# Performance work log

Hardware: AMD Instinct MI355X
Metric: run time of the kernel (lower is better)

Reference implementation:

```python
import jax, jax.numpy as jnp
import numpy as np

N_NODE, N_USER = 100000, 30000
N_REL, N_BASIS = 8, 30
EMB, OUT = 32, 32
E = 1600000
BATCH = 16384
H1, H2, H3 = 64, 32, 16
NEG_SLOPE = 0.2


def setup_inputs() -> dict:
    key = jax.random.key(0)
    ks = jax.random.split(key, 20)
    g = lambda k, shape: jax.random.normal(k, shape, dtype=jnp.float32) * 0.05
    inp = {
        "x_ids": jnp.arange(N_NODE, dtype=jnp.int64 if jax.config.jax_enable_x64 else jnp.int32),
        "edge_index": jax.random.randint(ks[0], (2, E), 0, N_NODE),
        "edge_type": jax.random.randint(ks[1], (E,), 0, N_REL),
        "users": jax.random.randint(ks[2], (BATCH,), 0, N_USER),
        "bundles": jax.random.randint(ks[3], (BATCH,), 0, N_NODE),
        # parameters
        "emb": g(ks[4], (N_NODE, EMB)),
        "basis": g(ks[5], (N_BASIS, EMB, OUT)),
        "weight": g(ks[6], (N_REL, N_BASIS)),
        "att": g(ks[7], (N_REL, 2 * OUT)),
        "root": g(ks[8], (EMB, OUT)),
        "bias": jnp.zeros((OUT,), jnp.float32),
        "W1": g(ks[9], (2 * OUT, H1)), "b1": jnp.zeros((H1,), jnp.float32),
        "W2": g(ks[10], (H1, H2)), "b2": jnp.zeros((H2,), jnp.float32),
        "W3": g(ks[11], (H2, H3)), "b3": jnp.zeros((H3,), jnp.float32),
        "Wo": g(ks[12], (H3, 1)), "bo": jnp.zeros((1,), jnp.float32),
    }
    return inp


def _tgcn_fwd(x_ids, edge_index, edge_type, users, bundles,
              emb, basis, weight, att, root, bias,
              W1, b1, W2, b2, W3, b3, Wo, bo):
    N = emb.shape[0]
    R = weight.shape[0]
    O = basis.shape[2]
    x = emb[x_ids]                                   # (N, F) embedding lookup
    # basis decomposition: (R, F, O)
    w = (weight @ basis.reshape(N_BASIS, -1)).reshape(R, EMB, O)
    # transform every node under every relation once, then gather per edge
    xh = jnp.einsum('nf,rfo->nro', x, w)             # (N, R, O)
    src, dst = edge_index[0], edge_index[1]          # j (source), i (target)
    h_i = xh[dst, edge_type]                         # (E, O)
    h_j = xh[src, edge_type]                         # (E, O)
    a = att[edge_type]                               # (E, 2O)
    alpha = (h_i * a[:, :O]).sum(-1) + (h_j * a[:, O:]).sum(-1)
    alpha = jax.nn.leaky_relu(alpha, NEG_SLOPE)
    # segment softmax keyed by (target node, relation)
    seg_key = dst * R + edge_type
    n_seg = N * R
    amax = jax.ops.segment_max(alpha, seg_key, num_segments=n_seg)
    ex = jnp.exp(alpha - amax[seg_key])
    denom = jax.ops.segment_sum(ex, seg_key, num_segments=n_seg)
    alpha = ex / (denom[seg_key] + 1e-16)
    # scatter-add weighted messages into target nodes
    agg = jax.ops.segment_sum(h_j * alpha[:, None], dst, num_segments=N)
    h = jax.nn.relu(agg + x @ root + bias)           # update + ReLU
    z = jnp.concatenate([h[users], h[bundles]], axis=1)  # (B, 2O)
    z = jax.nn.relu(z @ W1 + b1)
    z = jax.nn.relu(z @ W2 + b2)
    z = jax.nn.relu(z @ W3 + b3)
    return z @ Wo + bo                               # (B, 1) logits


def reference(x_ids, edge_index, edge_type, users, bundles,
              emb, basis, weight, att, root, bias,
              W1, b1, W2, b2, W3, b3, Wo, bo):
    return _tgcn_fwd(x_ids, edge_index, edge_type, users, bundles,
                     emb, basis, weight, att, root, bias,
                     W1, b1, W2, b2, W3, b3, Wo, bo)
```

## Files before the change

### kernel.cpp

```cpp
#include <hip/hip_runtime.h>
#include <hip/hip_bf16.h>

#define N_NODE 100000
#define N_REL  8
#define EMB    32
#define OUT    32
#define N_BASIS 30
#define E_EDGE 1600000
#define BATCH  16384
#define H1 64
#define H2 32
#define H3 16
#define NEG_SLOPE 0.2f

#define BSH   8
#define NBKT  391
#define BCAP  5120
#define PCH   2048

#define K5T   64

#define NPB   32
#define NTILES (N_NODE / NPB)
#define K1GRID 782
#define XSS   36
#define RTS   36


struct SortSmem {
    unsigned ent[BCAP];
    unsigned ent2[BCAP];
    unsigned hist[256], dbase[256], dcur[256], sc[256];
};
struct K1Smem {
    float xs[2][NPB * XSS];
    float rootsT[OUT * RTS];
    float was[16 * RTS];
    float biass[OUT];
};

__global__ __launch_bounds__(256) void k0f(const float* __restrict__ weight,
                                           const float* __restrict__ basis,
                                           const float* __restrict__ att,
                                           float* __restrict__ w,
                                           float* __restrict__ wa,
                                           unsigned* __restrict__ bcnt) {
    __shared__ float wl[N_REL * EMB * OUT];
    int t = threadIdx.x;
    for (int i = t; i < N_REL * EMB * OUT; i += 256) {
        int r = i >> 10, fo = i & 1023;
        float acc = 0.f;
        #pragma unroll
        for (int b = 0; b < N_BASIS; b++)
            acc = fmaf(weight[r * N_BASIS + b], basis[b * (EMB * OUT) + fo], acc);
        wl[i] = acc;
        w[i] = acc;
    }
    __syncthreads();
    for (int i = t; i < 512; i += 256) {
        int which = i >> 8, rf = i & 255, r = rf >> 5, f = rf & 31;
        const float* wrow = wl + (r * 32 + f) * 32;
        const float* arow = att + r * 64 + which * 32;
        float acc = 0.f;
        #pragma unroll
        for (int o = 0; o < 32; o++) acc = fmaf(wrow[o], arow[o], acc);
        wa[i] = acc;
    }
    for (int i = t; i < NBKT; i += 256) bcnt[i] = 0;
}

__device__ __forceinline__ void k1x_body(K1Smem& K, int bid0,
                                         const float* __restrict__ emb,
                                         const float* __restrict__ w,
                                         const float* __restrict__ wa,
                                         const float* __restrict__ root,
                                         const float* __restrict__ bias,
                                         unsigned short* __restrict__ xh,
                                         float* __restrict__ p_i,
                                         float* __restrict__ p_j,
                                         float* __restrict__ agg) {
    const int t = threadIdx.x;
    const int ro = t & 127;
    const int rhi = ro >> 5, olo = ro & 31;

    float wc0[EMB], wc1[EMB];
    #pragma unroll
    for (int f = 0; f < EMB; f++) {
        wc0[f] = w[rhi * 1024 + f * 32 + olo];
        wc1[f] = w[rhi * 1024 + 4096 + f * 32 + olo];
    }
    #pragma unroll
    for (int f = 0; f < EMB; f++) asm volatile("" : "+v"(wc0[f]), "+v"(wc1[f]));

    for (int i = t; i < EMB * OUT; i += 256) {
        int f = i >> 5, oo = i & 31;
        K.rootsT[oo * RTS + f] = root[i];
    }
    for (int i = t; i < 512; i += 256) {
        int which = i >> 8, r = (i >> 5) & 7, f = i & 31;
        K.was[(which * 8 + r) * RTS + f] = wa[i];
    }
    if (t < OUT) K.biass[t] = bias[t];

    const int sn = t >> 3, scn = t & 7;
    int tile = bid0;
    {
        float4 v = ((const float4*)(emb + (size_t)tile * NPB * EMB))[t];
        *(float4*)&K.xs[0][sn * XSS + scn * 4] = v;
    }
    __syncthreads();

    int buf = 0;
    for (; tile < NTILES; tile += K1GRID) {
        const int ntile = tile + K1GRID;
        const bool has = ntile < NTILES;
        float4 pf;
        if (has)
            pf = ((const float4*)(emb + (size_t)ntile * NPB * EMB))[t];

        const int n0 = tile * NPB;
        const float* xb = K.xs[buf];

        {
            const float4* xr = (const float4*)&xb[(t >> 3) * XSS];
            const float4* wi = (const float4*)&K.was[(t & 7) * RTS];
            const float4* wj = (const float4*)&K.was[(8 + (t & 7)) * RTS];
            float ai = 0.f, aj = 0.f;
            #pragma unroll
            for (int c = 0; c < 8; c++) {
                float4 xv = xr[c];
                float4 vi = wi[c], vj = wj[c];
                ai = fmaf(xv.x, vi.x, ai); ai = fmaf(xv.y, vi.y, ai);
                ai = fmaf(xv.z, vi.z, ai); ai = fmaf(xv.w, vi.w, ai);
                aj = fmaf(xv.x, vj.x, aj); aj = fmaf(xv.y, vj.y, aj);
                aj = fmaf(xv.z, vj.z, aj); aj = fmaf(xv.w, vj.w, aj);
            }
            p_i[n0 * N_REL + t] = ai;
            p_j[n0 * N_REL + t] = aj;
        }

        {
            const int o = t & 31, ng = t >> 5;
            const float4* rt = (const float4*)&K.rootsT[o * RTS];
            float4 r0 = rt[0], r1 = rt[1], r2 = rt[2], r3 = rt[3];
            float4 r4 = rt[4], r5 = rt[5], r6 = rt[6], r7 = rt[7];
            float bv = K.biass[o];
            #pragma unroll
            for (int q = 0; q < 4; q++) {
                int n = ng * 4 + q;
                const float4* xr = (const float4*)&xb[n * XSS];
                float g = bv;
                float4 xv;
                xv = xr[0]; g = fmaf(xv.x, r0.x, g); g = fmaf(xv.y, r0.y, g);
                            g = fmaf(xv.z, r0.z, g); g = fmaf(xv.w, r0.w, g);
                xv = xr[1]; g = fmaf(xv.x, r1.x, g); g = fmaf(xv.y, r1.y, g);
                            g = fmaf(xv.z, r1.z, g); g = fmaf(xv.w, r1.w, g);
                xv = xr[2]; g = fmaf(xv.x, r2.x, g); g = fmaf(xv.y, r2.y, g);
                            g = fmaf(xv.z, r2.z, g); g = fmaf(xv.w, r2.w, g);
                xv = xr[3]; g = fmaf(xv.x, r3.x, g); g = fmaf(xv.y, r3.y, g);
                            g = fmaf(xv.z, r3.z, g); g = fmaf(xv.w, r3.w, g);
                xv = xr[4]; g = fmaf(xv.x, r4.x, g); g = fmaf(xv.y, r4.y, g);
                            g = fmaf(xv.z, r4.z, g); g = fmaf(xv.w, r4.w, g);
                xv = xr[5]; g = fmaf(xv.x, r5.x, g); g = fmaf(xv.y, r5.y, g);
                            g = fmaf(xv.z, r5.z, g); g = fmaf(xv.w, r5.w, g);
                xv = xr[6]; g = fmaf(xv.x, r6.x, g); g = fmaf(xv.y, r6.y, g);
                            g = fmaf(xv.z, r6.z, g); g = fmaf(xv.w, r6.w, g);
                xv = xr[7]; g = fmaf(xv.x, r7.x, g); g = fmaf(xv.y, r7.y, g);
                            g = fmaf(xv.z, r7.z, g); g = fmaf(xv.w, r7.w, g);
                agg[(size_t)(n0 + n) * OUT + o] = g;
            }
        }

        {
            const int half = t >> 7;
            #pragma unroll 4
            for (int s = 0; s < 16; s++) {
                int n = 2 * s + half;
                const float4* xr = (const float4*)&xb[n * XSS];
                float a0 = 0.f, a1 = 0.f;
                #pragma unroll
                for (int c = 0; c < 8; c++) {
                    float4 xv = xr[c];
                    a0 = fmaf(xv.x, wc0[4 * c + 0], a0);
                    a0 = fmaf(xv.y, wc0[4 * c + 1], a0);
                    a0 = fmaf(xv.z, wc0[4 * c + 2], a0);
                    a0 = fmaf(xv.w, wc0[4 * c + 3], a0);
                    a1 = fmaf(xv.x, wc1[4 * c + 0], a1);
                    a1 = fmaf(xv.y, wc1[4 * c + 1], a1);
                    a1 = fmaf(xv.z, wc1[4 * c + 2], a1);
                    a1 = fmaf(xv.w, wc1[4 * c + 3], a1);
                }
                __hip_bfloat16 b0 = __float2bfloat16(a0);
                __hip_bfloat16 b1 = __float2bfloat16(a1);
                unsigned short* xp = xh + (size_t)(n0 + n) * 256;
                xp[ro]       = *(unsigned short*)&b0;
                xp[ro + 128] = *(unsigned short*)&b1;
            }
        }

        if (has)
            *(float4*)&K.xs[buf ^ 1][sn * XSS + scn * 4] = pf;
        __syncthreads();
        buf ^= 1;
    }
}

__device__ __forceinline__ void sort_body(SortSmem& S, int b,
                                          const unsigned* __restrict__ bcnt,
                                          const unsigned* __restrict__ part,
                                          int* __restrict__ payload,
                                          int* __restrict__ begp,
                                          int* __restrict__ endp) {
    int t = threadIdx.x;
    unsigned s0 = (unsigned)b * BCAP;
    int n = (int)bcnt[b];
    if (n > BCAP) n = BCAP;
    S.hist[t] = 0;
    __syncthreads();
    int n4 = n & ~3;
    for (int i = 4 * t; i < n4; i += 1024) {
        uint4 e4 = *(const uint4*)&part[s0 + i];
        S.ent[i + 0] = e4.x; atomicAdd(&S.hist[e4.x >> 20], 1u);
        S.ent[i + 1] = e4.y; atomicAdd(&S.hist[e4.y >> 20], 1u);
        S.ent[i + 2] = e4.z; atomicAdd(&S.hist[e4.z >> 20], 1u);
        S.ent[i + 3] = e4.w; atomicAdd(&S.hist[e4.w >> 20], 1u);
    }
    for (int i = n4 + t; i < n; i += 256) {
        unsigned e = part[s0 + i];
        S.ent[i] = e;
        atomicAdd(&S.hist[e >> 20], 1u);
    }
    __syncthreads();
    unsigned v = S.hist[t];
    S.sc[t] = v;
    __syncthreads();
    for (int off = 1; off < 256; off <<= 1) {
        unsigned y = (t >= off) ? S.sc[t - off] : 0u;
        __syncthreads();
        S.sc[t] += y;
        __syncthreads();
    }
    unsigned ex = S.sc[t] - v;
    S.dbase[t] = ex;
    S.dcur[t] = ex;
    __syncthreads();
    int d = (b << BSH) + t;
    if (d < N_NODE) {
        begp[d] = (int)(s0 + S.dbase[t]);
        endp[d] = (int)(s0 + S.dbase[t] + S.hist[t]);
    }
    for (int i = t; i < n; i += 256) {
        unsigned e = S.ent[i];
        unsigned pos = atomicAdd(&S.dcur[e >> 20], 1u);
        S.ent2[pos] = e & 0xFFFFFu;
    }
    __syncthreads();
    for (int i = 4 * t; i < n4; i += 1024) {
        uint4 o4 = { S.ent2[i + 0], S.ent2[i + 1], S.ent2[i + 2], S.ent2[i + 3] };
        *(uint4*)&payload[s0 + i] = o4;
    }
    for (int i = n4 + t; i < n; i += 256) payload[s0 + i] = (int)S.ent2[i];
}

__global__ __launch_bounds__(256) void k1x(const float* __restrict__ emb,
                                           const float* __restrict__ w,
                                           const float* __restrict__ wa,
                                           const float* __restrict__ root,
                                           const float* __restrict__ bias,
                                           unsigned short* __restrict__ xh,
                                           float* __restrict__ p_i,
                                           float* __restrict__ p_j,
                                           float* __restrict__ agg) {
    __shared__ K1Smem K;
    k1x_body(K, blockIdx.x, emb, w, wa, root, bias, xh, p_i, p_j, agg);
}

__global__ __launch_bounds__(256) void k_sort(const unsigned* __restrict__ bcnt,
                                              const unsigned* __restrict__ part,
                                              int* __restrict__ payload,
                                              int* __restrict__ begp,
                                              int* __restrict__ endp) {
    __shared__ SortSmem S;
    sort_body(S, blockIdx.x, bcnt, part, payload, begp, endp);
}

__global__ __launch_bounds__(256) void k_sx(const unsigned* __restrict__ bcnt,
                                            const unsigned* __restrict__ part,
                                            int* __restrict__ payload,
                                            int* __restrict__ begp,
                                            int* __restrict__ endp,
                                            const float* __restrict__ emb,
                                            const float* __restrict__ w,
                                            const float* __restrict__ wa,
                                            const float* __restrict__ root,
                                            const float* __restrict__ bias,
                                            unsigned short* __restrict__ xh,
                                            float* __restrict__ p_i,
                                            float* __restrict__ p_j,
                                            float* __restrict__ agg) {
    __shared__ union USmem { SortSmem s; K1Smem k; } u;
    if (blockIdx.x < K1GRID)
        k1x_body(u.k, blockIdx.x, emb, w, wa, root, bias, xh, p_i, p_j, agg);
    else
        sort_body(u.s, blockIdx.x - K1GRID, bcnt, part, payload, begp, endp);
}

__global__ __launch_bounds__(256) void k_part(const int* __restrict__ src,
                                              const int* __restrict__ dst,
                                              const int* __restrict__ et,
                                              unsigned* __restrict__ bcnt,
                                              unsigned* __restrict__ part) {
    __shared__ unsigned long long stage[PCH];
    __shared__ unsigned hist[NBKT], lbase[NBKT], lcur[NBKT], gbase[NBKT];
    __shared__ unsigned sc[256];
    int t = threadIdx.x;
    for (int i = t; i < NBKT; i += 256) hist[i] = 0;
    __syncthreads();
    int beg = blockIdx.x * PCH, end = min(beg + PCH, E_EDGE);
    int n = end - beg;
    int ng = n >> 2;
    int g0 = t, g1 = t + 256;
    bool has0 = g0 < ng, has1 = g1 < ng;
    int4 s0v = {}, d0v = {}, e0v = {}, s1v = {}, d1v = {}, e1v = {};
    if (has0) {
        s0v = *(const int4*)&src[beg + 4 * g0];
        d0v = *(const int4*)&dst[beg + 4 * g0];
        e0v = *(const int4*)&et[beg + 4 * g0];
    }
    if (has1) {
        s1v = *(const int4*)&src[beg + 4 * g1];
        d1v = *(const int4*)&dst[beg + 4 * g1];
        e1v = *(const int4*)&et[beg + 4 * g1];
    }
    if (has0) {
        atomicAdd(&hist[(unsigned)d0v.x >> BSH], 1u);
        atomicAdd(&hist[(unsigned)d0v.y >> BSH], 1u);
        atomicAdd(&hist[(unsigned)d0v.z >> BSH], 1u);
        atomicAdd(&hist[(unsigned)d0v.w >> BSH], 1u);
    }
    if (has1) {
        atomicAdd(&hist[(unsigned)d1v.x >> BSH], 1u);
        atomicAdd(&hist[(unsigned)d1v.y >> BSH], 1u);
        atomicAdd(&hist[(unsigned)d1v.z >> BSH], 1u);
        atomicAdd(&hist[(unsigned)d1v.w >> BSH], 1u);
    }
    __syncthreads();
    unsigned v0 = (2 * t < NBKT) ? hist[2 * t] : 0u;
    unsigned v1 = (2 * t + 1 < NBKT) ? hist[2 * t + 1] : 0u;
    unsigned s = v0 + v1;
    sc[t] = s;
    __syncthreads();
    for (int off = 1; off < 256; off <<= 1) {
        unsigned y = (t >= off) ? sc[t - off] : 0u;
        __syncthreads();
        sc[t] += y;
        __syncthreads();
    }
    unsigned ex = sc[t] - s;
    if (2 * t < NBKT)     { lbase[2 * t] = ex;          lcur[2 * t] = ex; }
    if (2 * t + 1 < NBKT) { lbase[2 * t + 1] = ex + v0; lcur[2 * t + 1] = ex + v0; }
    __syncthreads();
    #define K_PART_STAGE(dd, ss, ee) do {                                   \
        unsigned b_ = (unsigned)(dd) >> BSH;                                \
        unsigned ent_ = ((unsigned)((dd) & 255) << 20)                      \
                      | ((unsigned)(ss) << 3) | (unsigned)(ee);             \
        unsigned pos_ = atomicAdd(&lcur[b_], 1u);                           \
        stage[pos_] = ((unsigned long long)b_ << 32) | ent_; } while (0)
    if (has0) {
        K_PART_STAGE(d0v.x, s0v.x, e0v.x);
        K_PART_STAGE(d0v.y, s0v.y, e0v.y);
        K_PART_STAGE(d0v.z, s0v.z, e0v.z);
        K_PART_STAGE(d0v.w, s0v.w, e0v.w);
    }
    if (has1) {
        K_PART_STAGE(d1v.x, s1v.x, e1v.x);
        K_PART_STAGE(d1v.y, s1v.y, e1v.y);
        K_PART_STAGE(d1v.z, s1v.z, e1v.z);
        K_PART_STAGE(d1v.w, s1v.w, e1v.w);
    }
    #undef K_PART_STAGE
    __syncthreads();
    for (int i = t; i < NBKT; i += 256)
        if (hist[i]) gbase[i] = atomicAdd(&bcnt[i], hist[i]);
    __syncthreads();
    for (int i = t; i < n; i += 256) {
        unsigned long long s64 = stage[i];
        unsigned b = (unsigned)(s64 >> 32);
        unsigned ent = (unsigned)s64;
        part[b * BCAP + gbase[b] + (i - lbase[b])] = ent;
    }
}

__global__ __launch_bounds__(256) void k_agg(const int* __restrict__ begp,
                                             const int* __restrict__ endp,
                                             const int* __restrict__ payload,
                                             const float* __restrict__ p_i,
                                             const float* __restrict__ p_j,
                                             const unsigned short* __restrict__ xh,
                                             float* __restrict__ agg,
                                             int d0, int d1) {
    int d = d0 + blockIdx.x * 4 + (threadIdx.x >> 6);
    if (d >= d1) return;
    const int lane = threadIdx.x & 63;
    const int h = lane >> 5;
    const int o = lane & 31;
    const int beg = begp[d], end = endp[d];
    const int cnt = end - beg;
    if (cnt == 0) return;

    float pid[8];
    #pragma unroll
    for (int k = 0; k < 8; k++) pid[k] = p_i[(d << 3) | k];

    if (cnt <= 64) {
        int sr = 0, r = 0; float ev = 0.f;
        if (lane < cnt) {
            sr = payload[beg + lane];
            r = sr & 7;
            float pi = pid[0];
            #pragma unroll
            for (int k = 1; k < 8; k++) pi = (r == k) ? pid[k] : pi;
            float a = pi + p_j[sr];
            a = (a >= 0.f) ? a : NEG_SLOPE * a;
            ev = __expf(a);
        }
        float sex[8];
        #pragma unroll
        for (int k = 0; k < 8; k++) sex[k] = (r == k) ? ev : 0.f;
        #pragma unroll
        for (int k = 0; k < 8; k++) {
            #pragma unroll
            for (int m = 1; m <= 32; m <<= 1) sex[k] += __shfl_xor(sex[k], m, 64);
        }
        float de = sex[0];
        #pragma unroll
        for (int k = 1; k < 8; k++) de = (r == k) ? sex[k] : de;
        float al = ev / (de + 1e-16f);

        float w0 = 0.f, w1 = 0.f, w2 = 0.f, w3 = 0.f;
        for (int j0 = 0; j0 < cnt; j0 += 8) {
            float b0 = __shfl(al, j0 + h,     64);
            float b1 = __shfl(al, j0 + 2 + h, 64);
            float b2 = __shfl(al, j0 + 4 + h, 64);
            float b3 = __shfl(al, j0 + 6 + h, 64);
            int t0 = payload[beg + j0 + h]     & 0xFFFFF;
            int t1 = payload[beg + j0 + 2 + h] & 0xFFFFF;
            int t2 = payload[beg + j0 + 4 + h] & 0xFFFFF;
            int t3 = payload[beg + j0 + 6 + h] & 0xFFFFF;
            float x0 = __uint_as_float((unsigned)xh[((unsigned)t0 << 5) + o] << 16);
            float x1 = __uint_as_float((unsigned)xh[((unsigned)t1 << 5) + o] << 16);
            float x2 = __uint_as_float((unsigned)xh[((unsigned)t2 << 5) + o] << 16);
            float x3 = __uint_as_float((unsigned)xh[((unsigned)t3 << 5) + o] << 16);
            w0 = fmaf(b0, x0, w0); w1 = fmaf(b1, x1, w1);
            w2 = fmaf(b2, x2, w2); w3 = fmaf(b3, x3, w3);
        }
        float vv = (w0 + w1) + (w2 + w3);
        vv += __shfl_xor(vv, 32, 64);
        if (h == 0) agg[(size_t)d * OUT + o] += vv;
        return;
    }

    float sex[8] = {0.f,0.f,0.f,0.f,0.f,0.f,0.f,0.f};
    for (int i = beg + lane; i < end; i += 64) {
        int sr = payload[i];
        int r = sr & 7;
        float pi = pid[0];
        #pragma unroll
        for (int k = 1; k < 8; k++) pi = (r == k) ? pid[k] : pi;
        float a = pi + p_j[sr];
        a = (a >= 0.f) ? a : NEG_SLOPE * a;
        float ev = __expf(a);
        #pragma unroll
        for (int k = 0; k < 8; k++) sex[k] += (r == k) ? ev : 0.f;
    }
    #pragma unroll
    for (int k = 0; k < 8; k++) {
        #pragma unroll
        for (int m = 1; m <= 32; m <<= 1) sex[k] += __shfl_xor(sex[k], m, 64);
    }
    float v0 = 0.f;
    for (int c = beg; c < end; c += 64) {
        int i = c + lane;
        int sr = 0; float al = 0.f;
        if (i < end) {
            sr = payload[i];
            int r = sr & 7;
            float pi = pid[0];
            #pragma unroll
            for (int k = 1; k < 8; k++) pi = (r == k) ? pid[k] : pi;
            float a = pi + p_j[sr];
            a = (a >= 0.f) ? a : NEG_SLOPE * a;
            float ev = __expf(a);
            float de = sex[0];
            #pragma unroll
            for (int k = 1; k < 8; k++) de = (r == k) ? sex[k] : de;
            al = ev / (de + 1e-16f);
        }
        int m = min(64, end - c);
        for (int j0 = 0; j0 < m; j0 += 2) {
            int e0 = j0 + h;
            float a0 = __shfl(al, e0, 64); int s0 = __shfl(sr, e0, 64);
            if (e0 < m) {
                float xv = __uint_as_float((unsigned)xh[((unsigned)s0 << 5) + o] << 16);
                v0 = fmaf(a0, xv, v0);
            }
        }
    }
    float vv = v0;
    vv += __shfl_xor(vv, 32, 64);
    if (h == 0) agg[(size_t)d * OUT + o] += vv;
}

__global__ __launch_bounds__(K5T, 1) void k5_mlp(const int* __restrict__ users,
                                                 const int* __restrict__ bundles,
                                                 const float* __restrict__ agg,
                                                 const float* __restrict__ W1,
                                                 const float* __restrict__ b1,
                                                 const float* __restrict__ W2,
                                                 const float* __restrict__ b2,
                                                 const float* __restrict__ W3,
                                                 const float* __restrict__ b3,
                                                 const float* __restrict__ Wo,
                                                 const float* __restrict__ bo,
                                                 float* __restrict__ out) {
    __shared__ float4 W1s[2 * OUT * H1 / 4];
    __shared__ float4 W2s[H1 * H2 / 4];
    __shared__ float4 W3s[H2 * H3 / 4];
    __shared__ float b1s[H1], b2s[H2], b3s[H3], Wos[H3];
    __shared__ float bos;
    __shared__ float zs[K5T * 65];
    __shared__ float h1s[K5T * 65];
    const int t = threadIdx.x;

    const float4* W14 = (const float4*)W1;
    const float4* W24 = (const float4*)W2;
    const float4* W34 = (const float4*)W3;
    for (int i = t; i < 1024; i += K5T) W1s[i] = W14[i];
    for (int i = t; i < 512; i += K5T) W2s[i] = W24[i];
    for (int i = t; i < 128; i += K5T) W3s[i] = W34[i];
    if (t < H2) b2s[t] = b2[t];
    if (t < H3) { b3s[t] = b3[t]; Wos[t] = Wo[t]; }
    if (t < H1) b1s[t] = b1[t];
    if (t == 0) bos = bo[0];

    const int item = blockIdx.x * K5T + t;
    const int u = users[item], v = bundles[item];
    const float4* av = (const float4*)agg;
    float* zrow = &zs[t * 65];
    float* h1row = &h1s[t * 65];

    #pragma unroll
    for (int c = 0; c < 8; c++) {
        float4 x = av[(size_t)u * 8 + c];
        zrow[4 * c + 0] = fmaxf(x.x, 0.f); zrow[4 * c + 1] = fmaxf(x.y, 0.f);
        zrow[4 * c + 2] = fmaxf(x.z, 0.f); zrow[4 * c + 3] = fmaxf(x.w, 0.f);
    }
    #pragma unroll
    for (int c = 0; c < 8; c++) {
        float4 x = av[(size_t)v * 8 + c];
        zrow[32 + 4 * c + 0] = fmaxf(x.x, 0.f); zrow[32 + 4 * c + 1] = fmaxf(x.y, 0.f);
        zrow[32 + 4 * c + 2] = fmaxf(x.z, 0.f); zrow[32 + 4 * c + 3] = fmaxf(x.w, 0.f);
    }
    __syncthreads();

    #pragma unroll 4
    for (int j4 = 0; j4 < 16; j4++) {
        float a0 = b1s[4 * j4 + 0], a1 = b1s[4 * j4 + 1];
        float a2 = b1s[4 * j4 + 2], a3 = b1s[4 * j4 + 3];
        #pragma unroll 16
        for (int k = 0; k < 2 * OUT; k++) {
            float zk = zrow[k];
            float4 wv = W1s[k * 16 + j4];
            a0 = fmaf(zk, wv.x, a0); a1 = fmaf(zk, wv.y, a1);
            a2 = fmaf(zk, wv.z, a2); a3 = fmaf(zk, wv.w, a3);
        }
        h1row[4 * j4 + 0] = fmaxf(a0, 0.f); h1row[4 * j4 + 1] = fmaxf(a1, 0.f);
        h1row[4 * j4 + 2] = fmaxf(a2, 0.f); h1row[4 * j4 + 3] = fmaxf(a3, 0.f);
    }

    #pragma unroll 4
    for (int j4 = 0; j4 < 8; j4++) {
        float a0 = b2s[4 * j4 + 0], a1 = b2s[4 * j4 + 1];
        float a2 = b2s[4 * j4 + 2], a3 = b2s[4 * j4 + 3];
        #pragma unroll 16
        for (int k = 0; k < H1; k++) {
            float hk = h1row[k];
            float4 wv = W2s[k * 8 + j4];
            a0 = fmaf(hk, wv.x, a0); a1 = fmaf(hk, wv.y, a1);
            a2 = fmaf(hk, wv.z, a2); a3 = fmaf(hk, wv.w, a3);
        }
        zrow[4 * j4 + 0] = fmaxf(a0, 0.f); zrow[4 * j4 + 1] = fmaxf(a1, 0.f);
        zrow[4 * j4 + 2] = fmaxf(a2, 0.f); zrow[4 * j4 + 3] = fmaxf(a3, 0.f);
    }

    float h3v[16];
    #pragma unroll
    for (int j4 = 0; j4 < 4; j4++) {
        float a0 = b3s[4 * j4 + 0], a1 = b3s[4 * j4 + 1];
        float a2 = b3s[4 * j4 + 2], a3 = b3s[4 * j4 + 3];
        #pragma unroll 16
        for (int k = 0; k < H2; k++) {
            float hk = zrow[k];
            float4 wv = W3s[k * 4 + j4];
            a0 = fmaf(hk, wv.x, a0); a1 = fmaf(hk, wv.y, a1);
            a2 = fmaf(hk, wv.z, a2); a3 = fmaf(hk, wv.w, a3);
        }
        h3v[4 * j4 + 0] = fmaxf(a0, 0.f); h3v[4 * j4 + 1] = fmaxf(a1, 0.f);
        h3v[4 * j4 + 2] = fmaxf(a2, 0.f); h3v[4 * j4 + 3] = fmaxf(a3, 0.f);
    }

    float acc = bos;
    #pragma unroll
    for (int k = 0; k < H3; k++) acc = fmaf(h3v[k], Wos[k], acc);
    out[item] = acc;
}

extern "C" void kernel_launch(void* const* d_in, const int* in_sizes, int n_in,
                              void* d_out, int out_size, void* d_ws, size_t ws_size,
                              hipStream_t stream) {
    (void)in_sizes; (void)n_in; (void)out_size;
    const int*   eidx   = (const int*)d_in[1];
    const int*   etype  = (const int*)d_in[2];
    const int*   users  = (const int*)d_in[3];
    const int*   bund   = (const int*)d_in[4];
    const float* emb    = (const float*)d_in[5];
    const float* basis  = (const float*)d_in[6];
    const float* weight = (const float*)d_in[7];
    const float* att    = (const float*)d_in[8];
    const float* root   = (const float*)d_in[9];
    const float* bias   = (const float*)d_in[10];
    const float* W1 = (const float*)d_in[11]; const float* b1 = (const float*)d_in[12];
    const float* W2 = (const float*)d_in[13]; const float* b2 = (const float*)d_in[14];
    const float* W3 = (const float*)d_in[15]; const float* b3 = (const float*)d_in[16];
    const float* Wo = (const float*)d_in[17]; const float* bo = (const float*)d_in[18];
    float* out = (float*)d_out;

    const int* src = eidx;
    const int* dst = eidx + E_EDGE;

    float* ws       = (float*)d_ws;
    float* w        = ws;
    float* wa       = w + N_REL * EMB * OUT;
    unsigned short* xh = (unsigned short*)(wa + 512);
    float* p_i      = (float*)(xh + (size_t)N_NODE * 256);
    float* p_j      = p_i + N_NODE * N_REL;
    float* agg      = p_j + N_NODE * N_REL;
    int*   payload  = (int*)(agg + (size_t)N_NODE * OUT);
    int*   begp     = payload + (size_t)NBKT * BCAP;
    int*   endp     = begp + N_NODE;
    unsigned* bcnt  = (unsigned*)(endp + N_NODE);
    unsigned* part_sep = bcnt + 512;
    size_t needed = (size_t)((char*)(part_sep + (size_t)NBKT * BCAP) - (char*)d_ws);

    const bool fused = ws_size >= needed;
    unsigned* part = fused ? part_sep : (unsigned*)agg;

    k0f<<<1, 256, 0, stream>>>(weight, basis, att, w, wa, bcnt);
    k_part<<<(E_EDGE + PCH - 1) / PCH, 256, 0, stream>>>(src, dst, etype, bcnt, part);
    if (fused) {
        k_sx<<<K1GRID + NBKT, 256, 0, stream>>>(bcnt, part, payload, begp, endp,
                                                emb, w, wa, root, bias,
                                                xh, p_i, p_j, agg);
    } else {
        k_sort<<<NBKT, 256, 0, stream>>>(bcnt, part, payload, begp, endp);
        k1x<<<K1GRID, 256, 0, stream>>>(emb, w, wa, root, bias, xh, p_i, p_j, agg);
    }
    k_agg<<<N_NODE / 4, 256, 0, stream>>>(begp, endp, payload, p_i, p_j, xh, agg,
                                          0, N_NODE);
    k5_mlp<<<BATCH / K5T, K5T, 0, stream>>>(users, bund, agg, W1, b1, W2, b2, W3, b3,
                                            Wo, bo, out);
}
```

Measured before the change: 300.9 us.

## Split attention softmax into per-bucket alpha kernel before weighted aggregation

Keeps the local destination index in the sorted payload and adds a k_alpha kernel that computes softmax weights per bucket, using shared-memory atomics for the per-(node,relation) denominators and writing the alphas to a workspace buffer. A simplified k_agg_pv then only gathers xh rows and accumulates alpha-weighted messages. This takes the exp, select chains and wave shuffle reductions out of the per-node aggregation loop. In exchange it costs an extra kernel launch, an extra write and read of one float per edge, and needs a larger workspace, falling back to the old path when the workspace is too small.

```diff
diff --git a/kernel.cpp b/kernel.cpp
--- a/kernel.cpp
+++ b/kernel.cpp
@@ -252,7 +252,7 @@
     for (int i = t; i < n; i += 256) {
         unsigned e = S.ent[i];
         unsigned pos = atomicAdd(&S.dcur[e >> 20], 1u);
-        S.ent2[pos] = e & 0xFFFFFu;
+        S.ent2[pos] = e;
     }
     __syncthreads();
     for (int i = 4 * t; i < n4; i += 1024) {
@@ -305,6 +305,79 @@
         sort_body(u.s, blockIdx.x - K1GRID, bcnt, part, payload, begp, endp);
 }
 
+__global__ __launch_bounds__(256) void k_alpha(const unsigned* __restrict__ bcnt,
+                                               const int* __restrict__ payload,
+                                               const float* __restrict__ p_i,
+                                               const float* __restrict__ p_j,
+                                               float* __restrict__ alphas) {
+    __shared__ float evs[BCAP];
+    __shared__ unsigned short bins[BCAP];
+    __shared__ float den[256 * N_REL];
+    __shared__ float pis[256 * N_REL];
+    const int t = threadIdx.x, b = blockIdx.x;
+    const unsigned s0 = (unsigned)b * BCAP;
+    int n = (int)bcnt[b];
+    if (n > BCAP) n = BCAP;
+    const int gbase = (b << BSH) * N_REL;
+    for (int i = t; i < 256 * N_REL; i += 256) {
+        den[i] = 0.f;
+        int g = gbase + i;
+        pis[i] = (g < N_NODE * N_REL) ? p_i[g] : 0.f;
+    }
+    __syncthreads();
+    for (int i = t; i < n; i += 256) {
+        unsigned e = (unsigned)payload[s0 + i];
+        unsigned sr = e & 0xFFFFFu;
+        unsigned bin = ((e >> 20) << 3) | (sr & 7u);
+        float a = pis[bin] + p_j[sr];
+        a = (a >= 0.f) ? a : NEG_SLOPE * a;
+        float ev = __expf(a);
+        evs[i] = ev;
+        bins[i] = (unsigned short)bin;
+        atomicAdd(&den[bin], ev);
+    }
+    __syncthreads();
+    for (int i = t; i < n; i += 256)
+        alphas[s0 + i] = evs[i] / (den[bins[i]] + 1e-16f);
+}
+
+__global__ __launch_bounds__(256) void k_agg_pv(const int* __restrict__ begp,
+                                                const int* __restrict__ endp,
+                                                const int* __restrict__ payload,
+                                                const float* __restrict__ alphas,
+                                                const unsigned short* __restrict__ xh,
+                                                float* __restrict__ agg) {
+    const int d = blockIdx.x * 4 + (threadIdx.x >> 6);
+    const int lane = threadIdx.x & 63;
+    const int h = lane >> 5;
+    const int o = lane & 31;
+    const int beg = begp[d], end = endp[d];
+    const int cnt = end - beg;
+    if (cnt == 0) return;
+
+    float w0 = 0.f, w1 = 0.f, w2 = 0.f, w3 = 0.f;
+    for (int j0 = 0; j0 < cnt; j0 += 8) {
+        const int i0 = beg + j0 + h, i1 = i0 + 2, i2 = i0 + 4, i3 = i0 + 6;
+        float b0 = (i0 < end) ? alphas[i0] : 0.f;
+        float b1 = (i1 < end) ? alphas[i1] : 0.f;
+        float b2 = (i2 < end) ? alphas[i2] : 0.f;
+        float b3 = (i3 < end) ? alphas[i3] : 0.f;
+        int t0 = payload[i0] & 0xFFFFF;
+        int t1 = payload[i1] & 0xFFFFF;
+        int t2 = payload[i2] & 0xFFFFF;
+        int t3 = payload[i3] & 0xFFFFF;
+        float x0 = __uint_as_float((unsigned)xh[((unsigned)t0 << 5) + o] << 16);
+        float x1 = __uint_as_float((unsigned)xh[((unsigned)t1 << 5) + o] << 16);
+        float x2 = __uint_as_float((unsigned)xh[((unsigned)t2 << 5) + o] << 16);
+        float x3 = __uint_as_float((unsigned)xh[((unsigned)t3 << 5) + o] << 16);
+        w0 = fmaf(b0, x0, w0); w1 = fmaf(b1, x1, w1);
+        w2 = fmaf(b2, x2, w2); w3 = fmaf(b3, x3, w3);
+    }
+    float vv = (w0 + w1) + (w2 + w3);
+    vv += __shfl_xor(vv, 32, 64);
+    if (h == 0) agg[(size_t)d * OUT + o] += vv;
+}
+
 __global__ __launch_bounds__(256) void k_part(const int* __restrict__ src,
                                               const int* __restrict__ dst,
                                               const int* __restrict__ et,
@@ -415,7 +488,7 @@
     if (cnt <= 64) {
         int sr = 0, r = 0; float ev = 0.f;
         if (lane < cnt) {
-            sr = payload[beg + lane];
+            sr = payload[beg + lane] & 0xFFFFF;
             r = sr & 7;
             float pi = pid[0];
             #pragma unroll
@@ -462,7 +535,7 @@
 
     float sex[8] = {0.f,0.f,0.f,0.f,0.f,0.f,0.f,0.f};
     for (int i = beg + lane; i < end; i += 64) {
-        int sr = payload[i];
+        int sr = payload[i] & 0xFFFFF;
         int r = sr & 7;
         float pi = pid[0];
         #pragma unroll
@@ -483,7 +556,7 @@
         int i = c + lane;
         int sr = 0; float al = 0.f;
         if (i < end) {
-            sr = payload[i];
+            sr = payload[i] & 0xFFFFF;
             int r = sr & 7;
             float pi = pid[0];
             #pragma unroll
@@ -650,14 +723,17 @@
     int*   endp     = begp + N_NODE;
     unsigned* bcnt  = (unsigned*)(endp + N_NODE);
     unsigned* part_sep = bcnt + 512;
-    size_t needed = (size_t)((char*)(part_sep + (size_t)NBKT * BCAP) - (char*)d_ws);
-
-    const bool fused = ws_size >= needed;
-    unsigned* part = fused ? part_sep : (unsigned*)agg;
+    float* alphas   = (float*)(part_sep + (size_t)NBKT * BCAP);
+    size_t needed_mid  = (size_t)((char*)alphas - (char*)d_ws);
+    size_t needed_full = (size_t)((char*)(alphas + (size_t)NBKT * BCAP) - (char*)d_ws);
+
+    const bool full = ws_size >= needed_full;
+    const bool mid  = ws_size >= needed_mid;
+    unsigned* part = mid ? part_sep : (unsigned*)agg;
 
     k0f<<<1, 256, 0, stream>>>(weight, basis, att, w, wa, bcnt);
     k_part<<<(E_EDGE + PCH - 1) / PCH, 256, 0, stream>>>(src, dst, etype, bcnt, part);
-    if (fused) {
+    if (mid) {
         k_sx<<<K1GRID + NBKT, 256, 0, stream>>>(bcnt, part, payload, begp, endp,
                                                 emb, w, wa, root, bias,
                                                 xh, p_i, p_j, agg);
@@ -665,8 +741,14 @@
         k_sort<<<NBKT, 256, 0, stream>>>(bcnt, part, payload, begp, endp);
         k1x<<<K1GRID, 256, 0, stream>>>(emb, w, wa, root, bias, xh, p_i, p_j, agg);
     }
-    k_agg<<<N_NODE / 4, 256, 0, stream>>>(begp, endp, payload, p_i, p_j, xh, agg,
-                                          0, N_NODE);
+    if (full) {
+        k_alpha<<<NBKT, 256, 0, stream>>>(bcnt, payload, p_i, p_j, alphas);
+        k_agg_pv<<<N_NODE / 4, 256, 0, stream>>>(begp, endp, payload, alphas,
+                                                 xh, agg);
+    } else {
+        k_agg<<<N_NODE / 4, 256, 0, stream>>>(begp, endp, payload, p_i, p_j, xh,
+                                              agg, 0, N_NODE);
+    }
     k5_mlp<<<BATCH / K5T, K5T, 0, stream>>>(users, bund, agg, W1, b1, W2, b2, W3, b3,
                                             Wo, bo, out);
 }
```

New measurement: 301.4 us. No clear change (+0.2%).

## Replace per-node aggregation with per-bucket kernel using shared-memory softmax

Applied to the files above, without the earlier changes.

Sorted payload entries now keep the local destination index in their upper bits. A new per-bucket kernel uses this to compute edge attention exponents once, accumulate per-(node, relation) denominators with shared-memory atomics, and normalise in shared memory. Its gather then uses paired bf16 dword loads across 16-lane groups. This removes the per-node two-pass recomputation of exponents and the 8-way shuffle reductions of the old per-node kernel, at the cost of one block per half-bucket handling up to BCAP edges and fewer, larger blocks.

```diff
diff --git a/kernel.cpp b/kernel.cpp
--- a/kernel.cpp
+++ b/kernel.cpp
@@ -252,7 +252,7 @@
     for (int i = t; i < n; i += 256) {
         unsigned e = S.ent[i];
         unsigned pos = atomicAdd(&S.dcur[e >> 20], 1u);
-        S.ent2[pos] = e & 0xFFFFFu;
+        S.ent2[pos] = e;
     }
     __syncthreads();
     for (int i = 4 * t; i < n4; i += 1024) {
@@ -305,6 +305,95 @@
         sort_body(u.s, blockIdx.x - K1GRID, bcnt, part, payload, begp, endp);
 }
 
+__global__ __launch_bounds__(256) void k_bpv(const unsigned* __restrict__ bcnt,
+                                             const int* __restrict__ begp,
+                                             const int* __restrict__ endp,
+                                             const int* __restrict__ payload,
+                                             const float* __restrict__ p_i,
+                                             const float* __restrict__ p_j,
+                                             const unsigned short* __restrict__ xh,
+                                             float* __restrict__ agg) {
+    __shared__ float evs[BCAP];
+    __shared__ unsigned short bins[BCAP];
+    __shared__ float den[128 * N_REL];
+    __shared__ float pis[128 * N_REL];
+    __shared__ int begs[128], ends[128];
+    const int t = threadIdx.x;
+    const int b = blockIdx.x >> 1, half = blockIdx.x & 1;
+    const int d0 = (b << BSH) + (half << 7);
+    const unsigned s0 = (unsigned)b * BCAP;
+    int nb = (int)bcnt[b];
+    if (nb > BCAP) nb = BCAP;
+    const int dmid = (b << BSH) + 128;
+    const int start   = (half == 0) ? (int)s0 : begp[dmid];
+    const int endSlot = (half == 0) ? begp[dmid] : (int)s0 + nb;
+    const int nh = endSlot - start;
+
+    if (t < 128) {
+        int d = d0 + t;
+        begs[t] = (d < N_NODE) ? begp[d] : 0;
+        ends[t] = (d < N_NODE) ? endp[d] : 0;
+    }
+    for (int i = t; i < 128 * N_REL; i += 256) {
+        den[i] = 0.f;
+        int g = d0 * N_REL + i;
+        pis[i] = (g < N_NODE * N_REL) ? p_i[g] : 0.f;
+    }
+    __syncthreads();
+
+    for (int i = t; i < nh; i += 256) {
+        unsigned e = (unsigned)payload[start + i];
+        unsigned sr = e & 0xFFFFFu;
+        unsigned bin = (((e >> 20) & 255u) - (unsigned)(half << 7)) * 8u + (sr & 7u);
+        float a = pis[bin] + p_j[sr];
+        a = (a >= 0.f) ? a : NEG_SLOPE * a;
+        float ev = __expf(a);
+        evs[i] = ev;
+        bins[i] = (unsigned short)bin;
+        atomicAdd(&den[bin], ev);
+    }
+    __syncthreads();
+    for (int i = t; i < nh; i += 256)
+        evs[i] = evs[i] / (den[bins[i]] + 1e-16f);
+    __syncthreads();
+
+    const int wv = t >> 6, L = t & 63;
+    const int g16 = L >> 4;
+    const int o2 = (L & 15) * 2;
+    for (int k = wv; k < 128; k += 4) {
+        int d = d0 + k;
+        if (d >= N_NODE) break;
+        const int beg = begs[k];
+        const int cnt = ends[k] - beg;
+        if (cnt == 0) continue;
+        float a0 = 0.f, a1 = 0.f, c0 = 0.f, c1 = 0.f;
+        for (int e0 = 0; e0 < cnt; e0 += 8) {
+            int eA = e0 + g16, eB = e0 + 4 + g16;
+            int iA = beg + ((eA < cnt) ? eA : 0);
+            int iB = beg + ((eB < cnt) ? eB : 0);
+            float alA = (eA < cnt) ? evs[iA - start] : 0.f;
+            float alB = (eB < cnt) ? evs[iB - start] : 0.f;
+            unsigned srA = (unsigned)payload[iA] & 0xFFFFFu;
+            unsigned srB = (unsigned)payload[iB] & 0xFFFFFu;
+            unsigned dwA = *(const unsigned*)&xh[(srA << 5) + o2];
+            unsigned dwB = *(const unsigned*)&xh[(srB << 5) + o2];
+            a0 = fmaf(alA, __uint_as_float((dwA & 0xFFFFu) << 16), a0);
+            a1 = fmaf(alA, __uint_as_float(dwA & 0xFFFF0000u), a1);
+            c0 = fmaf(alB, __uint_as_float((dwB & 0xFFFFu) << 16), c0);
+            c1 = fmaf(alB, __uint_as_float(dwB & 0xFFFF0000u), c1);
+        }
+        a0 += c0; a1 += c1;
+        a0 += __shfl_xor(a0, 16, 64); a0 += __shfl_xor(a0, 32, 64);
+        a1 += __shfl_xor(a1, 16, 64); a1 += __shfl_xor(a1, 32, 64);
+        if (L < 16) {
+            float* ap = &agg[(size_t)d * OUT + o2];
+            float2 cur = *(float2*)ap;
+            cur.x += a0; cur.y += a1;
+            *(float2*)ap = cur;
+        }
+    }
+}
+
 __global__ __launch_bounds__(256) void k_part(const int* __restrict__ src,
                                               const int* __restrict__ dst,
                                               const int* __restrict__ et,
@@ -415,7 +504,7 @@
     if (cnt <= 64) {
         int sr = 0, r = 0; float ev = 0.f;
         if (lane < cnt) {
-            sr = payload[beg + lane];
+            sr = payload[beg + lane] & 0xFFFFF;
             r = sr & 7;
             float pi = pid[0];
             #pragma unroll
@@ -462,7 +551,7 @@
 
     float sex[8] = {0.f,0.f,0.f,0.f,0.f,0.f,0.f,0.f};
     for (int i = beg + lane; i < end; i += 64) {
-        int sr = payload[i];
+        int sr = payload[i] & 0xFFFFF;
         int r = sr & 7;
         float pi = pid[0];
         #pragma unroll
@@ -483,7 +572,7 @@
         int i = c + lane;
         int sr = 0; float al = 0.f;
         if (i < end) {
-            sr = payload[i];
+            sr = payload[i] & 0xFFFFF;
             int r = sr & 7;
             float pi = pid[0];
             #pragma unroll
@@ -650,23 +739,25 @@
     int*   endp     = begp + N_NODE;
     unsigned* bcnt  = (unsigned*)(endp + N_NODE);
     unsigned* part_sep = bcnt + 512;
-    size_t needed = (size_t)((char*)(part_sep + (size_t)NBKT * BCAP) - (char*)d_ws);
-
-    const bool fused = ws_size >= needed;
-    unsigned* part = fused ? part_sep : (unsigned*)agg;
+    size_t needed_mid = (size_t)((char*)(part_sep + (size_t)NBKT * BCAP) - (char*)d_ws);
+
+    const bool mid = ws_size >= needed_mid;
+    unsigned* part = mid ? part_sep : (unsigned*)agg;
 
     k0f<<<1, 256, 0, stream>>>(weight, basis, att, w, wa, bcnt);
     k_part<<<(E_EDGE + PCH - 1) / PCH, 256, 0, stream>>>(src, dst, etype, bcnt, part);
-    if (fused) {
+    if (mid) {
         k_sx<<<K1GRID + NBKT, 256, 0, stream>>>(bcnt, part, payload, begp, endp,
                                                 emb, w, wa, root, bias,
                                                 xh, p_i, p_j, agg);
+        k_bpv<<<2 * NBKT, 256, 0, stream>>>(bcnt, begp, endp, payload,
+                                            p_i, p_j, xh, agg);
     } else {
         k_sort<<<NBKT, 256, 0, stream>>>(bcnt, part, payload, begp, endp);
         k1x<<<K1GRID, 256, 0, stream>>>(emb, w, wa, root, bias, xh, p_i, p_j, agg);
-    }
-    k_agg<<<N_NODE / 4, 256, 0, stream>>>(begp, endp, payload, p_i, p_j, xh, agg,
-                                          0, N_NODE);
+        k_agg<<<N_NODE / 4, 256, 0, stream>>>(begp, endp, payload, p_i, p_j, xh,
+                                              agg, 0, N_NODE);
+    }
     k5_mlp<<<BATCH / K5T, K5T, 0, stream>>>(users, bund, agg, W1, b1, W2, b2, W3, b3,
                                             Wo, bo, out);
 }
```

After: 323.7 us. 1.08x slower.
